# Kernel optimization log

Hardware: AMD Instinct MI355X
Metric: run time of the kernel (lower is better)

## Reference

```python
import jax, jax.numpy as jnp
import numpy as np

N, L, D = 100000, 4, 64          # nodes, gcn layers, emb_dim
B, S = 16384, 32                 # links, intersection-set size
INP, RELD, NREL, NDIST = 32, 32, 200, 11
PSD = L * D                      # param_set_dim = 256


def setup_inputs() -> dict:
    key = jax.random.key(0)
    ks = jax.random.split(key, 16)
    return {
        "node_repr": jax.random.normal(ks[0], (N, L, D), jnp.float32),
        "node_feat": jax.random.normal(ks[1], (N, INP), jnp.float32),
        "head_idx": jax.random.randint(ks[2], (B,), 0, N, jnp.int32),
        "rel_idx": jax.random.randint(ks[3], (B,), 0, NREL, jnp.int32),
        "tail_idx": jax.random.randint(ks[4], (B,), 0, N, jnp.int32),
        "dist": jax.random.randint(ks[5], (B,), 0, NDIST, jnp.int32),
        "inter_count": jax.random.randint(ks[6], (B, S), 0, N, jnp.int32),
        "rel_emb": jax.random.normal(ks[7], (NREL, RELD), jnp.float32),
        "dist_emb": jax.random.normal(ks[8], (NDIST, D), jnp.float32),
        "head_W": jax.random.normal(ks[9], (PSD + D, INP), jnp.float32) * 0.05,
        "head_b": jnp.zeros((INP,), jnp.float32),
        "tail_W": jax.random.normal(ks[10], (PSD + D, INP), jnp.float32) * 0.05,
        "tail_b": jnp.zeros((INP,), jnp.float32),
        "W1": jax.random.normal(ks[11], (2 * PSD + RELD + 2 * INP + PSD, 64), jnp.float32) * 0.05,
        "b1": jnp.zeros((64,), jnp.float32),
        "W2": jax.random.normal(ks[12], (64, 32), jnp.float32) * 0.05,
        "b2": jnp.zeros((32,), jnp.float32),
        "W3": jax.random.normal(ks[13], (32, 1), jnp.float32) * 0.05,
        "b3": jnp.zeros((1,), jnp.float32),
    }


def reference(node_repr, node_feat, head_idx, rel_idx, tail_idx, dist, inter_count,
              rel_emb, dist_emb, head_W, head_b, tail_W, tail_b,
              W1, b1, W2, b2, W3, b3):
    flat = node_repr.reshape(node_repr.shape[0], -1)           # [N, PSD]
    head_repr = flat[head_idx]                                 # [B, PSD]
    tail_repr = flat[tail_idx]                                 # [B, PSD]
    rel_repr = rel_emb[rel_idx]                                # [B, RELD]

    # masked gather + mean over the intersection set (-1 entries masked out)
    sign = jnp.sign(inter_count + 1).astype(flat.dtype)        # [B, S]
    mid = flat[jnp.abs(inter_count)] * sign[:, :, None]        # [B, S, PSD]
    mid = mid.sum(axis=1)                                      # [B, PSD]
    cnt = jnp.clip(jnp.sum(inter_count != -1, axis=1), 1, None)
    mid_repr = mid / cnt[:, None].astype(flat.dtype)

    dist_repr = dist_emb[dist]                                 # [B, D]

    md = jnp.concatenate([mid_repr, dist_repr], axis=1)        # [B, PSD+D]
    head_pred = md @ head_W + head_b                           # [B, INP]
    tail_pred = md @ tail_W + tail_b
    head_init_feat = node_feat[head_idx]
    tail_init_feat = node_feat[tail_idx]

    g_rep = jnp.concatenate(
        [head_repr, tail_repr, rel_repr, mid_repr, head_init_feat, tail_init_feat], axis=1)
    h = jax.nn.relu(g_rep @ W1 + b1)
    h = jax.nn.relu(h @ W2 + b2)
    output = h @ W3 + b3                                       # [B, 1]
    return (output, head_pred, tail_pred, head_init_feat, tail_init_feat)
```

## Files before the change

kernel.cpp:

```cpp
#include <hip/hip_runtime.h>
#include <cstddef>
#include <cstdint>

typedef __bf16 bf16x8 __attribute__((ext_vector_type(8)));
typedef float  f32x4  __attribute__((ext_vector_type(4)));

#define NLINK 16
#define X_STRIDE 936
#define H1_STRIDE 66
#define WTC_ELEMS (128 * 928)
#define WTC_BYTES (WTC_ELEMS * 2)

__device__ __forceinline__ float b2f(unsigned short u) {
    unsigned int x = (unsigned int)u << 16;
    return __builtin_bit_cast(float, x);
}
__device__ __forceinline__ unsigned short f2b(float f) {
    unsigned int u = __builtin_bit_cast(unsigned int, f);
    u += 0x7FFFu + ((u >> 16) & 1u);
    return (unsigned short)(u >> 16);
}

__global__ void prep_weights(const float* __restrict__ W1,
                             const float* __restrict__ headW,
                             const float* __restrict__ tailW,
                             unsigned short* __restrict__ WTc) {
    const int n = blockIdx.x;
    for (int k = threadIdx.x; k < 928; k += blockDim.x) {
        float v = 0.f;
        if (n < 64) {
            if (k < 864) v = W1[(size_t)k * 64 + n];
        } else {
            const int c = (n < 96) ? (n - 64) : (n - 96);
            const float* W = (n < 96) ? headW : tailW;
            if (k >= 544 && k < 800)      v = W[(size_t)(k - 544) * 32 + c];
            else if (k >= 864 && k < 928) v = W[(size_t)(256 + (k - 864)) * 32 + c];
        }
        WTc[(size_t)n * 928 + k] = f2b(v);
    }
}

__device__ __forceinline__ bf16x8 gather_Bfrag(const float* __restrict__ W1,
                                               const float* __restrict__ hW,
                                               const float* __restrict__ tW,
                                               int n, int k0) {
    unsigned short r[8];
    if (n < 64) {
        #pragma unroll
        for (int j = 0; j < 8; ++j) {
            const int k = k0 + j;
            r[j] = (k < 864) ? f2b(W1[(size_t)k * 64 + n]) : (unsigned short)0;
        }
    } else {
        const float* W = (n < 96) ? hW : tW;
        const int c = (n < 96) ? (n - 64) : (n - 96);
        #pragma unroll
        for (int j = 0; j < 8; ++j) {
            const int k = k0 + j;
            float v = 0.f;
            if (k >= 544 && k < 800)      v = W[(size_t)(k - 544) * 32 + c];
            else if (k >= 864 && k < 928) v = W[(size_t)(256 + (k - 864)) * 32 + c];
            r[j] = f2b(v);
        }
    }
    unsigned short tmp[8];
    #pragma unroll
    for (int j = 0; j < 8; ++j) tmp[j] = r[j];
    return __builtin_bit_cast(bf16x8, *(const uint4*)tmp);
}

template <bool USE_WTC>
__global__ __launch_bounds__(256, 4) void fused_main(
    const float* __restrict__ node_repr,
    const float* __restrict__ node_feat,
    const int* __restrict__ head_idx,
    const int* __restrict__ rel_idx,
    const int* __restrict__ tail_idx,
    const int* __restrict__ dist,
    const int* __restrict__ inter,
    const float* __restrict__ rel_emb,
    const float* __restrict__ dist_emb,
    const float* __restrict__ b1p,
    const float* __restrict__ head_bp,
    const float* __restrict__ tail_bp,
    const float* __restrict__ W2p,
    const float* __restrict__ b2p,
    const float* __restrict__ W3p,
    const float* __restrict__ b3p,
    const unsigned short* __restrict__ WTc,
    const float* __restrict__ W1p,
    const float* __restrict__ headWp,
    const float* __restrict__ tailWp,
    float* __restrict__ out,
    int B)
{
    extern __shared__ char smem[];
    unsigned short* sX  = (unsigned short*)smem;
    unsigned short* sH1 = (unsigned short*)(smem + NLINK * X_STRIDE * 2);

    const int tid  = threadIdx.x;
    const int w    = tid >> 6;
    const int lane = tid & 63;
    const int g0   = blockIdx.x * NLINK;

    float* out0   = out;
    float* out_hp = out + B;
    float* out_tp = out + B + (size_t)B * 32;
    float* out_hf = out + B + (size_t)B * 64;
    float* out_tf = out + B + (size_t)B * 96;

    for (int li = 0; li < 4; ++li) {
        const int L = w * 4 + li;
        const int g = g0 + L;
        if (g >= B) continue;

        const int hidx = head_idx[g];
        const int tidx = tail_idx[g];
        const int ridx = rel_idx[g];
        const int didx = dist[g];
        const int c4 = lane * 4;

        float4 hr = *(const float4*)(node_repr + (size_t)hidx * 256 + c4);
        float4 tr = *(const float4*)(node_repr + (size_t)tidx * 256 + c4);
        ushort4 hb; hb.x = f2b(hr.x); hb.y = f2b(hr.y); hb.z = f2b(hr.z); hb.w = f2b(hr.w);
        ushort4 tb; tb.x = f2b(tr.x); tb.y = f2b(tr.y); tb.z = f2b(tr.z); tb.w = f2b(tr.w);
        *(ushort4*)(sX + (size_t)L * X_STRIDE + c4)       = hb;
        *(ushort4*)(sX + (size_t)L * X_STRIDE + 256 + c4) = tb;

        float a0 = 0.f, a1 = 0.f, a2 = 0.f, a3 = 0.f;
        int cnt = 0;
        const int* icp = inter + (size_t)g * 32;
        #pragma unroll
        for (int s = 0; s < 32; ++s) {
            const int ic = icp[s];
            const int idx = (ic >= 0) ? ic : -ic;
            const float sg = (ic == -1) ? 0.f : ((ic >= 0) ? 1.f : -1.f);
            float4 v = *(const float4*)(node_repr + (size_t)idx * 256 + c4);
            a0 += sg * v.x; a1 += sg * v.y;
            a2 += sg * v.z; a3 += sg * v.w;
            cnt += (ic != -1) ? 1 : 0;
        }
        const float inv = 1.0f / (float)(cnt > 0 ? cnt : 1);
        ushort4 mv;
        mv.x = f2b(a0 * inv); mv.y = f2b(a1 * inv);
        mv.z = f2b(a2 * inv); mv.w = f2b(a3 * inv);
        *(ushort4*)(sX + (size_t)L * X_STRIDE + 544 + c4) = mv;

        if (lane < 32) {
            const float hf = node_feat[(size_t)hidx * 32 + lane];
            const float tf = node_feat[(size_t)tidx * 32 + lane];
            const float rv = rel_emb[(size_t)ridx * 32 + lane];
            sX[(size_t)L * X_STRIDE + 800 + lane] = f2b(hf);
            sX[(size_t)L * X_STRIDE + 832 + lane] = f2b(tf);
            sX[(size_t)L * X_STRIDE + 512 + lane] = f2b(rv);
            out_hf[(size_t)g * 32 + lane] = hf;
            out_tf[(size_t)g * 32 + lane] = tf;
        }
        sX[(size_t)L * X_STRIDE + 864 + lane] = f2b(dist_emb[(size_t)didx * 64 + lane]);
    }
    __syncthreads();

    const int col16 = lane & 15;
    const int quad  = lane >> 4;
    const int n0    = w * 32;

    f32x4 accv[2] = {{0.f,0.f,0.f,0.f},{0.f,0.f,0.f,0.f}};

    const unsigned short* aP = sX + (size_t)col16 * X_STRIDE + quad * 8;

    if (USE_WTC) {
        const unsigned short* bP0 = WTc + (size_t)(n0 +  0 + col16) * 928 + quad * 8;
        const unsigned short* bP1 = WTc + (size_t)(n0 + 16 + col16) * 928 + quad * 8;
        for (int ks = 0; ks < 29; ++ks) {
            const bf16x8 af = __builtin_bit_cast(bf16x8, *(const uint4*)(aP + ks * 32));
            bf16x8 b0 = __builtin_bit_cast(bf16x8, *(const uint4*)(bP0 + ks * 32));
            bf16x8 b1 = __builtin_bit_cast(bf16x8, *(const uint4*)(bP1 + ks * 32));
            accv[0] = __builtin_amdgcn_mfma_f32_16x16x32_bf16(af, b0, accv[0], 0, 0, 0);
            accv[1] = __builtin_amdgcn_mfma_f32_16x16x32_bf16(af, b1, accv[1], 0, 0, 0);
        }
    } else {
        for (int ks = 0; ks < 29; ++ks) {
            const int k0 = ks * 32 + quad * 8;
            const bf16x8 af = __builtin_bit_cast(bf16x8, *(const uint4*)(aP + ks * 32));
            bf16x8 b0 = gather_Bfrag(W1p, headWp, tailWp, n0 +  0 + col16, k0);
            bf16x8 b1 = gather_Bfrag(W1p, headWp, tailWp, n0 + 16 + col16, k0);
            accv[0] = __builtin_amdgcn_mfma_f32_16x16x32_bf16(af, b0, accv[0], 0, 0, 0);
            accv[1] = __builtin_amdgcn_mfma_f32_16x16x32_bf16(af, b1, accv[1], 0, 0, 0);
        }
    }

    if (n0 < 64) {
        #pragma unroll
        for (int t = 0; t < 2; ++t) {
            const int n = n0 + t * 16 + col16;
            const float bias = b1p[n];
            #pragma unroll
            for (int r = 0; r < 4; ++r) {
                float v = accv[t][r] + bias;
                v = v > 0.f ? v : 0.f;
                sH1[(size_t)(quad * 4 + r) * H1_STRIDE + n] = f2b(v);
            }
        }
    } else {
        const bool isH = (n0 < 96);
        const float* bp = isH ? head_bp : tail_bp;
        float* dst = isH ? out_hp : out_tp;
        #pragma unroll
        for (int t = 0; t < 2; ++t) {
            const int c = (n0 - (isH ? 64 : 96)) + t * 16 + col16;
            const float bias = bp[c];
            #pragma unroll
            for (int r = 0; r < 4; ++r) {
                const int m = g0 + quad * 4 + r;
                if (m < B) dst[(size_t)m * 32 + c] = accv[t][r] + bias;
            }
        }
    }
    __syncthreads();

    const int half = lane >> 5;
    const int c    = lane & 31;
    const float w3v = W3p[c];
    const float b2v = b2p[c];
    const float b3v = b3p[0];
    #pragma unroll
    for (int pass = 0; pass < 2; ++pass) {
        const int L = w * 4 + pass * 2 + half;
        float acc = 0.f;
        #pragma unroll 8
        for (int k = 0; k < 64; ++k)
            acc += b2f(sH1[(size_t)L * H1_STRIDE + k]) * W2p[(size_t)k * 32 + c];
        const float h2 = fmaxf(acc + b2v, 0.f);
        float p = h2 * w3v;
        p += __shfl_xor(p, 16);
        p += __shfl_xor(p, 8);
        p += __shfl_xor(p, 4);
        p += __shfl_xor(p, 2);
        p += __shfl_xor(p, 1);
        if (c == 0 && (g0 + L) < B) out0[g0 + L] = p + b3v;
    }
}

extern "C" void kernel_launch(void* const* d_in, const int* in_sizes, int n_in,
                              void* d_out, int out_size, void* d_ws, size_t ws_size,
                              hipStream_t stream) {
    const float* node_repr = (const float*)d_in[0];
    const float* node_feat = (const float*)d_in[1];
    const int* head_idx = (const int*)d_in[2];
    const int* rel_idx  = (const int*)d_in[3];
    const int* tail_idx = (const int*)d_in[4];
    const int* dist     = (const int*)d_in[5];
    const int* inter    = (const int*)d_in[6];
    const float* rel_emb  = (const float*)d_in[7];
    const float* dist_emb = (const float*)d_in[8];
    const float* head_W   = (const float*)d_in[9];
    const float* head_b   = (const float*)d_in[10];
    const float* tail_W   = (const float*)d_in[11];
    const float* tail_b   = (const float*)d_in[12];
    const float* W1       = (const float*)d_in[13];
    const float* b1       = (const float*)d_in[14];
    const float* W2       = (const float*)d_in[15];
    const float* b2       = (const float*)d_in[16];
    const float* W3       = (const float*)d_in[17];
    const float* b3       = (const float*)d_in[18];

    const int B = in_sizes[2];
    float* out = (float*)d_out;

    const int grid = (B + NLINK - 1) / NLINK;
    const size_t lds = (size_t)NLINK * X_STRIDE * 2 + (size_t)NLINK * H1_STRIDE * 2;

    if (ws_size >= (size_t)WTC_BYTES) {
        unsigned short* WTc = (unsigned short*)d_ws;
        hipLaunchKernelGGL(prep_weights, dim3(128), dim3(256), 0, stream,
                           W1, head_W, tail_W, WTc);
        hipLaunchKernelGGL((fused_main<true>), dim3(grid), dim3(256), lds, stream,
                           node_repr, node_feat, head_idx, rel_idx, tail_idx, dist, inter,
                           rel_emb, dist_emb, b1, head_b, tail_b, W2, b2, W3, b3,
                           WTc, W1, head_W, tail_W, out, B);
    } else {
        hipLaunchKernelGGL((fused_main<false>), dim3(grid), dim3(256), lds, stream,
                           node_repr, node_feat, head_idx, rel_idx, tail_idx, dist, inter,
                           rel_emb, dist_emb, b1, head_b, tail_b, W2, b2, W3, b3,
                           (const unsigned short*)nullptr, W1, head_W, tail_W, out, B);
    }
}
```

Baseline: 260.5 us.

## Use 8 waves per block with one link pair and one MFMA tile per wave

Result: no change. 257.6 us (-1.1%).

```diff
diff --git a/kernel.cpp b/kernel.cpp
--- a/kernel.cpp
+++ b/kernel.cpp
@@ -70,7 +70,7 @@
 }
 
 template <bool USE_WTC>
-__global__ __launch_bounds__(256, 4) void fused_main(
+__global__ __launch_bounds__(512, 8) void fused_main(
     const float* __restrict__ node_repr,
     const float* __restrict__ node_feat,
     const int* __restrict__ head_idx,
@@ -109,8 +109,9 @@
     float* out_hf = out + B + (size_t)B * 64;
     float* out_tf = out + B + (size_t)B * 96;
 
-    for (int li = 0; li < 4; ++li) {
-        const int L = w * 4 + li;
+    #pragma unroll
+    for (int li = 0; li < 2; ++li) {
+        const int L = w * 2 + li;
         const int g = g0 + L;
         if (g >= B) continue;
 
@@ -162,58 +163,48 @@
 
     const int col16 = lane & 15;
     const int quad  = lane >> 4;
-    const int n0    = w * 32;
-
-    f32x4 accv[2] = {{0.f,0.f,0.f,0.f},{0.f,0.f,0.f,0.f}};
+    const int n0    = w * 16;
+
+    f32x4 acc = {0.f, 0.f, 0.f, 0.f};
 
     const unsigned short* aP = sX + (size_t)col16 * X_STRIDE + quad * 8;
 
     if (USE_WTC) {
-        const unsigned short* bP0 = WTc + (size_t)(n0 +  0 + col16) * 928 + quad * 8;
-        const unsigned short* bP1 = WTc + (size_t)(n0 + 16 + col16) * 928 + quad * 8;
+        const unsigned short* bP = WTc + (size_t)(n0 + col16) * 928 + quad * 8;
+        #pragma unroll
         for (int ks = 0; ks < 29; ++ks) {
             const bf16x8 af = __builtin_bit_cast(bf16x8, *(const uint4*)(aP + ks * 32));
-            bf16x8 b0 = __builtin_bit_cast(bf16x8, *(const uint4*)(bP0 + ks * 32));
-            bf16x8 b1 = __builtin_bit_cast(bf16x8, *(const uint4*)(bP1 + ks * 32));
-            accv[0] = __builtin_amdgcn_mfma_f32_16x16x32_bf16(af, b0, accv[0], 0, 0, 0);
-            accv[1] = __builtin_amdgcn_mfma_f32_16x16x32_bf16(af, b1, accv[1], 0, 0, 0);
+            const bf16x8 bf = __builtin_bit_cast(bf16x8, *(const uint4*)(bP + ks * 32));
+            acc = __builtin_amdgcn_mfma_f32_16x16x32_bf16(af, bf, acc, 0, 0, 0);
         }
     } else {
         for (int ks = 0; ks < 29; ++ks) {
             const int k0 = ks * 32 + quad * 8;
             const bf16x8 af = __builtin_bit_cast(bf16x8, *(const uint4*)(aP + ks * 32));
-            bf16x8 b0 = gather_Bfrag(W1p, headWp, tailWp, n0 +  0 + col16, k0);
-            bf16x8 b1 = gather_Bfrag(W1p, headWp, tailWp, n0 + 16 + col16, k0);
-            accv[0] = __builtin_amdgcn_mfma_f32_16x16x32_bf16(af, b0, accv[0], 0, 0, 0);
-            accv[1] = __builtin_amdgcn_mfma_f32_16x16x32_bf16(af, b1, accv[1], 0, 0, 0);
+            const bf16x8 bf = gather_Bfrag(W1p, headWp, tailWp, n0 + col16, k0);
+            acc = __builtin_amdgcn_mfma_f32_16x16x32_bf16(af, bf, acc, 0, 0, 0);
         }
     }
 
     if (n0 < 64) {
-        #pragma unroll
-        for (int t = 0; t < 2; ++t) {
-            const int n = n0 + t * 16 + col16;
-            const float bias = b1p[n];
-            #pragma unroll
-            for (int r = 0; r < 4; ++r) {
-                float v = accv[t][r] + bias;
-                v = v > 0.f ? v : 0.f;
-                sH1[(size_t)(quad * 4 + r) * H1_STRIDE + n] = f2b(v);
-            }
+        const int n = n0 + col16;
+        const float bias = b1p[n];
+        #pragma unroll
+        for (int r = 0; r < 4; ++r) {
+            float v = acc[r] + bias;
+            v = v > 0.f ? v : 0.f;
+            sH1[(size_t)(quad * 4 + r) * H1_STRIDE + n] = f2b(v);
         }
     } else {
         const bool isH = (n0 < 96);
         const float* bp = isH ? head_bp : tail_bp;
         float* dst = isH ? out_hp : out_tp;
-        #pragma unroll
-        for (int t = 0; t < 2; ++t) {
-            const int c = (n0 - (isH ? 64 : 96)) + t * 16 + col16;
-            const float bias = bp[c];
-            #pragma unroll
-            for (int r = 0; r < 4; ++r) {
-                const int m = g0 + quad * 4 + r;
-                if (m < B) dst[(size_t)m * 32 + c] = accv[t][r] + bias;
-            }
+        const int c = (n0 - (isH ? 64 : 96)) + col16;
+        const float bias = bp[c];
+        #pragma unroll
+        for (int r = 0; r < 4; ++r) {
+            const int m = g0 + quad * 4 + r;
+            if (m < B) dst[(size_t)m * 32 + c] = acc[r] + bias;
         }
     }
     __syncthreads();
@@ -223,14 +214,13 @@
     const float w3v = W3p[c];
     const float b2v = b2p[c];
     const float b3v = b3p[0];
-    #pragma unroll
-    for (int pass = 0; pass < 2; ++pass) {
-        const int L = w * 4 + pass * 2 + half;
-        float acc = 0.f;
+    {
+        const int L = w * 2 + half;
+        float accs = 0.f;
         #pragma unroll 8
         for (int k = 0; k < 64; ++k)
-            acc += b2f(sH1[(size_t)L * H1_STRIDE + k]) * W2p[(size_t)k * 32 + c];
-        const float h2 = fmaxf(acc + b2v, 0.f);
+            accs += b2f(sH1[(size_t)L * H1_STRIDE + k]) * W2p[(size_t)k * 32 + c];
+        const float h2 = fmaxf(accs + b2v, 0.f);
         float p = h2 * w3v;
         p += __shfl_xor(p, 16);
         p += __shfl_xor(p, 8);
@@ -274,12 +264,12 @@
         unsigned short* WTc = (unsigned short*)d_ws;
         hipLaunchKernelGGL(prep_weights, dim3(128), dim3(256), 0, stream,
                            W1, head_W, tail_W, WTc);
-        hipLaunchKernelGGL((fused_main<true>), dim3(grid), dim3(256), lds, stream,
+        hipLaunchKernelGGL((fused_main<true>), dim3(grid), dim3(512), lds, stream,
                            node_repr, node_feat, head_idx, rel_idx, tail_idx, dist, inter,
                            rel_emb, dist_emb, b1, head_b, tail_b, W2, b2, W3, b3,
                            WTc, W1, head_W, tail_W, out, B);
     } else {
-        hipLaunchKernelGGL((fused_main<false>), dim3(grid), dim3(256), lds, stream,
+        hipLaunchKernelGGL((fused_main<false>), dim3(grid), dim3(512), lds, stream,
                            node_repr, node_feat, head_idx, rel_idx, tail_idx, dist, inter,
                            rel_emb, dist_emb, b1, head_b, tail_b, W2, b2, W3, b3,
                            (const unsigned short*)nullptr, W1, head_W, tail_W, out, B);
```
